# Kernel optimization log

Hardware: AMD Instinct MI355X
Metric: run time of the kernel (lower is better)

The kernel has to match this reference:

```python
import jax, jax.numpy as jnp
from jax import lax
import numpy as np

HEADS, SAMPLES = 4, 8
B, C, D, H, W = 1, 64, 16, 64, 64
HD = C // HEADS  # head_dim = 16
BN_EPS = 1e-5


def conv3d(x, w, b=None, pad=0):
    out = lax.conv_general_dilated(
        x, w, (1, 1, 1), [(pad, pad)] * 3,
        dimension_numbers=("NCDHW", "OIDHW", "NCDHW"))
    if b is not None:
        out = out + b[None, :, None, None, None]
    return out


def trilinear_sample(vol, grid):
    # vol: [Dv,Hv,Wv,Cc]; grid: [...,3] with torch grid_sample semantics:
    # grid[...,0] -> x (W axis), grid[...,1] -> y (H axis), grid[...,2] -> z (D axis)
    # align_corners=True, padding_mode='border'. Returns [..., Cc].
    Dv, Hv, Wv, _ = vol.shape
    ix = (grid[..., 0] + 1.0) * 0.5 * (Wv - 1)
    iy = (grid[..., 1] + 1.0) * 0.5 * (Hv - 1)
    iz = (grid[..., 2] + 1.0) * 0.5 * (Dv - 1)
    x0 = jnp.floor(ix); y0 = jnp.floor(iy); z0 = jnp.floor(iz)
    wx = (ix - x0)[..., None]; wy = (iy - y0)[..., None]; wz = (iz - z0)[..., None]
    x0i = jnp.clip(x0.astype(jnp.int32), 0, Wv - 1); x1i = jnp.clip(x0i + 1, 0, Wv - 1)
    y0i = jnp.clip(y0.astype(jnp.int32), 0, Hv - 1); y1i = jnp.clip(y0i + 1, 0, Hv - 1)
    z0i = jnp.clip(z0.astype(jnp.int32), 0, Dv - 1); z1i = jnp.clip(z0i + 1, 0, Dv - 1)
    g = lambda z, y, x: vol[z, y, x]
    out = (g(z0i, y0i, x0i) * (1 - wz) * (1 - wy) * (1 - wx)
           + g(z0i, y0i, x1i) * (1 - wz) * (1 - wy) * wx
           + g(z0i, y1i, x0i) * (1 - wz) * wy * (1 - wx)
           + g(z0i, y1i, x1i) * (1 - wz) * wy * wx
           + g(z1i, y0i, x0i) * wz * (1 - wy) * (1 - wx)
           + g(z1i, y0i, x1i) * wz * (1 - wy) * wx
           + g(z1i, y1i, x0i) * wz * wy * (1 - wx)
           + g(z1i, y1i, x1i) * wz * wy * wx)
    return out


def t_deform(feat_prev, feat_curr, p):
    b, c, d, h, w = feat_curr.shape
    kv = conv3d(feat_prev, p["kv_w"], p["kv_b"])          # [B,2C,D,H,W]
    q = conv3d(feat_curr, p["q_w"], p["q_b"])              # [B,C,D,H,W]
    # offset branch: conv3x3 -> GELU(exact) -> conv3x3(no bias) -> tanh
    o = conv3d(feat_curr, p["off1_w"], p["off1_b"], pad=1)
    o = jax.nn.gelu(o, approximate=False)
    o = jnp.tanh(conv3d(o, p["off2_w"], None, pad=1))      # [B,M*S*3,D,H,W]
    off = o.reshape(b, HEADS, SAMPLES, 3, d, h, w).transpose(0, 1, 4, 5, 6, 2, 3)  # [B,M,D,H,W,S,3]
    zz, yy, xx = jnp.meshgrid(jnp.linspace(-1, 1, d), jnp.linspace(-1, 1, h),
                              jnp.linspace(-1, 1, w), indexing="ij")
    base = jnp.stack((zz, yy, xx), axis=-1).astype(feat_curr.dtype)  # [D,H,W,3]
    scale = jnp.array([d, h, w], dtype=feat_curr.dtype)
    grid = base[None, None, :, :, :, None, :] + off / scale
    grid = jnp.clip(grid, -1.0, 1.0)
    grid = grid.transpose(0, 1, 5, 2, 3, 4, 6).reshape(b * HEADS, SAMPLES, d, h, w, 3)
    # channels-last per (batch,head) volume; avoids torch's explicit repeat over samples
    vols = kv.reshape(b, HEADS, 2 * HD, d, h, w).transpose(0, 1, 3, 4, 5, 2)
    vols = vols.reshape(b * HEADS, d, h, w, 2 * HD)
    sampled = jax.vmap(trilinear_sample)(vols, grid)        # [B*M,S,D,H,W,2*HD]
    sampled = sampled.reshape(b, HEADS, SAMPLES, d, h, w, 2 * HD)
    key, value = sampled[..., :HD], sampled[..., HD:]
    qh = q.reshape(b, HEADS, HD, d, h, w) * (HD ** -0.5)
    attn = jnp.einsum("bmcdhw,bmsdhwc->bmsdhw", qh, key)
    attn = jax.nn.softmax(attn, axis=2)
    fused = jnp.einsum("bmsdhw,bmsdhwc->bmcdhw", attn, value).reshape(b, c, d, h, w)
    out = conv3d(fused, p["out_w"], p["out_b"])
    # BatchNorm3d (eval: running stats) + ReLU
    inv = lax.rsqrt(p["bn_var"] + BN_EPS)
    out = (out - p["bn_mean"][None, :, None, None, None]) * (inv * p["bn_gamma"])[None, :, None, None, None] \
          + p["bn_beta"][None, :, None, None, None]
    return jax.nn.relu(out)


def setup_inputs() -> dict:
    key = jax.random.key(0)
    ks = jax.random.split(key, 16)
    r = lambda k, shp, s=0.05: (jax.random.normal(k, shp, dtype=jnp.float32) * s)
    return {
        "mid_feat": jax.random.normal(ks[0], (B, C, D, H, W), dtype=jnp.float32),
        "occ_feat": jax.random.normal(ks[1], (B, C, D, H, W), dtype=jnp.float32),
        "prev_feat": jax.random.normal(ks[2], (B, C, D, H, W), dtype=jnp.float32),
        "off1_w": r(ks[3], (C, C, 3, 3, 3)), "off1_b": r(ks[4], (C,)),
        "off2_w": r(ks[5], (HEADS * SAMPLES * 3, C, 3, 3, 3)),
        "kv_w": r(ks[6], (2 * C, C, 1, 1, 1)), "kv_b": r(ks[7], (2 * C,)),
        "q_w": r(ks[8], (C, C, 1, 1, 1)), "q_b": r(ks[9], (C,)),
        "out_w": r(ks[10], (C, C, 1, 1, 1)), "out_b": r(ks[11], (C,)),
        "bn_gamma": jnp.ones((C,), jnp.float32), "bn_beta": jnp.zeros((C,), jnp.float32),
        "bn_mean": jnp.zeros((C,), jnp.float32), "bn_var": jnp.ones((C,), jnp.float32),
    }


def reference(mid_feat, occ_feat, prev_feat, off1_w, off1_b, off2_w, kv_w, kv_b,
              q_w, q_b, out_w, out_b, bn_gamma, bn_beta, bn_mean, bn_var):
    p = dict(off1_w=off1_w, off1_b=off1_b, off2_w=off2_w, kv_w=kv_w, kv_b=kv_b,
             q_w=q_w, q_b=q_b, out_w=out_w, out_b=out_b, bn_gamma=bn_gamma,
             bn_beta=bn_beta, bn_mean=bn_mean, bn_var=bn_var)
    d1 = t_deform(mid_feat, occ_feat, p)
    d2 = t_deform(mid_feat, prev_feat, p)
    return jnp.concatenate([mid_feat, d1, d2], axis=1)  # [B,3C,D,H,W]
```

## Files before the change

kernel.cpp:

```cpp
#include <hip/hip_runtime.h>
#include <math.h>

#define DD 16
#define HH 64
#define WW 64
#define VV (DD*HH*WW)
#define CC 64
#define NHEADS 4
#define NSAMP 8
#define HDIM 16

typedef unsigned int uint;
typedef unsigned short ushort;
typedef __attribute__((ext_vector_type(8))) short bf16x8;
typedef __attribute__((ext_vector_type(4))) float f32x4;

__device__ __forceinline__ float clampf(float v, float lo, float hi){ return fminf(fmaxf(v, lo), hi); }
__device__ __forceinline__ int imin(int a, int b){ return a < b ? a : b; }
__device__ __forceinline__ int imax(int a, int b){ return a > b ? a : b; }

__device__ __forceinline__ ushort f2bf(float f){
  uint u = __float_as_uint(f);
  uint r = (u + 0x7fffu + ((u>>16)&1u)) >> 16;
  return (ushort)r;
}
__device__ __forceinline__ uint packbf2(float a, float b){
  return (uint)f2bf(a) | ((uint)f2bf(b) << 16);
}
__device__ __forceinline__ float bflo(uint u){ return __uint_as_float(u << 16); }
__device__ __forceinline__ float bfhi(uint u){ return __uint_as_float(u & 0xffff0000u); }
__device__ __forceinline__ float bf2f(ushort u){ return __uint_as_float((uint)u << 16); }

__device__ __forceinline__ float dot8(uint4 k, const float* q){
  return q[0]*bflo(k.x)+q[1]*bfhi(k.x)+q[2]*bflo(k.y)+q[3]*bfhi(k.y)
       + q[4]*bflo(k.z)+q[5]*bfhi(k.z)+q[6]*bflo(k.w)+q[7]*bfhi(k.w);
}
__device__ __forceinline__ void acc8(uint4 u, float cw, float* val){
  val[0]+=cw*bflo(u.x); val[1]+=cw*bfhi(u.x);
  val[2]+=cw*bflo(u.y); val[3]+=cw*bfhi(u.y);
  val[4]+=cw*bflo(u.z); val[5]+=cw*bfhi(u.z);
  val[6]+=cw*bflo(u.w); val[7]+=cw*bfhi(u.w);
}

__global__ void repack_wmfma(const float* __restrict__ w, uint* __restrict__ o, int MG){
  int U = blockIdx.x*256 + threadIdx.x;
  int total = 54*MG*256;
  if (U >= total) return;
  int j2 = U & 3;
  int m  = (U>>2) & 15;
  int q  = (U>>6) & 3;
  int rest = U >> 8;
  int g = rest % MG;
  int s = rest / MG;
  int tap = s >> 1, h = s & 1;
  int co = g*16 + m;
  int ci = h*32 + q*8 + j2*2;
  int base = co*1728 + ci*27 + tap;
  o[U] = packbf2(w[base], w[base + 27]);
}
__global__ void repack_w1mfma(const float* __restrict__ w, uint* __restrict__ o, int MT){
  int U = blockIdx.x*256 + threadIdx.x;
  int total = 2*MT*256;
  if (U >= total) return;
  int j2 = U & 3;
  int lane = (U>>2) & 63;
  int frag = U >> 8;
  int mt = frag % MT;
  int ks = frag / MT;
  int q = lane >> 4, m = lane & 15;
  int co = mt*16 + m;
  int ci = ks*32 + q*8 + j2*2;
  o[U] = packbf2(w[co*CC + ci], w[co*CC + ci + 1]);
}

template<int CO, int EPI>
__global__ __launch_bounds__(256) void conv1_mfma(
    const float* __restrict__ xa, const float* __restrict__ xb,
    const uint* __restrict__ wA, const float* __restrict__ bias,
    void* __restrict__ outp)
{
  constexpr int MT = CO/16;
  constexpr int MW = MT/4;
  __shared__ ushort xt[64*72];
  int tid = threadIdx.x;
  int lane = tid & 63;
  int g = __builtin_amdgcn_readfirstlane(tid >> 6);
  int q = lane >> 4, n = lane & 15;
  int call = blockIdx.x >> 10;
  int v0 = (blockIdx.x & 1023) * 64;
  const float* x = call ? xb : xa;
  for (int it = tid; it < 64*32; it += 256){
    int vox = it & 63; int cp = it >> 6;
    float a = x[(size_t)(2*cp)*VV + v0 + vox];
    float b = x[(size_t)(2*cp+1)*VV + v0 + vox];
    *reinterpret_cast<uint*>(&xt[vox*72 + 2*cp]) = packbf2(a,b);
  }
  __syncthreads();
  f32x4 acc[MW][4];
  #pragma unroll
  for (int mw=0;mw<MW;mw++)
    #pragma unroll
    for (int nt=0;nt<4;nt++){ acc[mw][nt].x=0.f; acc[mw][nt].y=0.f; acc[mw][nt].z=0.f; acc[mw][nt].w=0.f; }
  const char* ldsb = reinterpret_cast<const char*>(xt);
  const char* wac  = reinterpret_cast<const char*>(wA);
  #pragma unroll
  for (int ks=0; ks<2; ks++){
    bf16x8 bfr[4];
    #pragma unroll
    for (int nt=0; nt<4; nt++)
      bfr[nt] = *reinterpret_cast<const bf16x8*>(ldsb + ((nt*16+n)*144 + q*16 + ks*64));
    #pragma unroll
    for (int mw=0; mw<MW; mw++){
      int mt = g*MW + mw;
      bf16x8 af = *reinterpret_cast<const bf16x8*>(wac + (size_t)((ks*MT + mt)*64 + lane)*16);
      #pragma unroll
      for (int nt=0; nt<4; nt++)
        acc[mw][nt] = __builtin_amdgcn_mfma_f32_16x16x32_bf16(af, bfr[nt], acc[mw][nt], 0, 0, 0);
    }
  }
  #pragma unroll
  for (int mw=0; mw<MW; mw++){
    int mt = g*MW + mw;
    int cob = mt*16 + q*4;
    #pragma unroll
    for (int nt=0; nt<4; nt++){
      int v = v0 + nt*16 + n;
      float r0 = acc[mw][nt].x + bias[cob+0];
      float r1 = acc[mw][nt].y + bias[cob+1];
      float r2 = acc[mw][nt].z + bias[cob+2];
      float r3 = acc[mw][nt].w + bias[cob+3];
      if (EPI == 0){
        int z = v >> 12, y = (v >> 6) & 63, xx = v & 63;
        int head = cob >> 5;
        uint* vols = (uint*)outp;
        uint2 pk; pk.x = packbf2(r0,r1); pk.y = packbf2(r2,r3);
        *reinterpret_cast<uint2*>(vols + ((size_t)head*VV + (size_t)(y*WW+xx)*DD + z)*16 + ((cob&31)>>1)) = pk;
      } else {
        ushort* ob = (ushort*)outp + (size_t)call*CC*VV;
        uint2 pk; pk.x = packbf2(r0*0.25f, r1*0.25f); pk.y = packbf2(r2*0.25f, r3*0.25f);
        *reinterpret_cast<uint2*>(ob + (size_t)v*64 + cob) = pk;
      }
    }
  }
}

template<int CO, int INPK, int OUTPK>
__global__ __launch_bounds__(256) void conv3_mfma(
    const float* __restrict__ xa, const float* __restrict__ xb,
    const uint* __restrict__ xpk,
    const uint* __restrict__ wA, const float* __restrict__ bias,
    void* __restrict__ outp)
{
  constexpr int MG = CO/16;
  constexpr int MROW = CO/32;
  __shared__ ushort xh[300*40];
  int tid = threadIdx.x;
  int lane = tid & 63;
  int w = __builtin_amdgcn_readfirstlane(tid >> 6);
  int q = lane >> 4, n = lane & 15;
  int bid = blockIdx.x;
  int xcd = bid & 7, islot = bid >> 3;
  int call = islot >> 7;
  int z = xcd*2 + ((islot >> 6) & 1);
  int rem = islot & 63;
  int by = (rem >> 3) << 3, bx = (rem & 7) << 3;

  const float* xin = call ? xb : xa;
  const uint* xinp = xpk + (size_t)call*32*VV;

  int mbase = (w & 1) * MROW;
  int np = w >> 1;
  int lo[2];
  #pragma unroll
  for (int nt=0;nt<2;nt++){
    int vox = (np*2+nt)*16 + n;
    lo[nt] = ((vox>>3)*10 + (vox&7))*80 + q*16;
  }
  f32x4 acc[MROW][2];
  #pragma unroll
  for (int mr=0;mr<MROW;mr++)
    #pragma unroll
    for (int nt=0;nt<2;nt++){ acc[mr][nt].x=0.f; acc[mr][nt].y=0.f; acc[mr][nt].z=0.f; acc[mr][nt].w=0.f; }

  const char* ldsb = reinterpret_cast<const char*>(xh);
  const char* wac  = reinterpret_cast<const char*>(wA);

  #pragma unroll 1
  for (int h=0; h<2; h++){
    if (h) __syncthreads();
    for (int it = tid; it < 2400; it += 256){
      int cg = it / 300; int pos = it - cg*300;
      int dz = pos/100; int r = pos - dz*100; int dy = r/10; int dxx = r - dy*10;
      int gz = z + dz - 1, gy = by + dy - 1, gx = bx + dxx - 1;
      bool ok = (gz>=0 && gz<DD && gy>=0 && gy<HH && gx>=0 && gx<WW);
      uint2 pk; pk.x = 0u; pk.y = 0u;
      if (ok){
        size_t gv = (size_t)((gz*HH+gy)*WW + gx);
        if (INPK){
          int cp0 = h*16 + cg*2;
          pk.x = xinp[(size_t)cp0*VV + gv];
          pk.y = xinp[(size_t)(cp0+1)*VV + gv];
        } else {
          int ci0 = h*32 + cg*4;
          float v0 = xin[(size_t)(ci0  )*VV + gv];
          float v1 = xin[(size_t)(ci0+1)*VV + gv];
          float v2 = xin[(size_t)(ci0+2)*VV + gv];
          float v3 = xin[(size_t)(ci0+3)*VV + gv];
          pk.x = packbf2(v0,v1); pk.y = packbf2(v2,v3);
        }
      }
      *reinterpret_cast<uint2*>(&xh[pos*40 + cg*4]) = pk;
    }
    __syncthreads();
    #pragma unroll 3
    for (int tap=0; tap<27; tap++){
      int dz = tap/9; int r9 = tap - dz*9; int dy = r9/3; int dxx = r9 - dy*3;
      int stepOff = (dz*100 + dy*10 + dxx)*80;
      int s = tap*2 + h;
      bf16x8 af[MROW];
      #pragma unroll
      for (int mr=0;mr<MROW;mr++)
        af[mr] = *reinterpret_cast<const bf16x8*>(wac + (size_t)((s*MG + mbase+mr)*64 + lane)*16);
      bf16x8 bf[2];
      #pragma unroll
      for (int nt=0;nt<2;nt++)
        bf[nt] = *reinterpret_cast<const bf16x8*>(ldsb + (lo[nt] + stepOff));
      #pragma unroll
      for (int mr=0;mr<MROW;mr++)
        #pragma unroll
        for (int nt=0;nt<2;nt++)
          acc[mr][nt] = __builtin_amdgcn_mfma_f32_16x16x32_bf16(af[mr], bf[nt], acc[mr][nt], 0, 0, 0);
    }
  }

  #pragma unroll
  for (int mr=0; mr<MROW; mr++){
    int cob = (mbase+mr)*16 + q*4;
    #pragma unroll
    for (int nt=0; nt<2; nt++){
      int vox = (np*2+nt)*16 + n;
      int vy = by + (vox>>3), vx = bx + (vox&8-1);
      vy = by + (vox>>3); vx = bx + (vox&7);
      size_t gv = (size_t)((z*HH + vy)*WW + vx);
      float r0 = acc[mr][nt].x, r1 = acc[mr][nt].y, r2 = acc[mr][nt].z, r3 = acc[mr][nt].w;
      if (OUTPK == 1){
        r0 += bias[cob+0]; r1 += bias[cob+1]; r2 += bias[cob+2]; r3 += bias[cob+3];
        r0 = 0.5f*r0*(1.f + erff(r0*0.70710678118654752f));
        r1 = 0.5f*r1*(1.f + erff(r1*0.70710678118654752f));
        r2 = 0.5f*r2*(1.f + erff(r2*0.70710678118654752f));
        r3 = 0.5f*r3*(1.f + erff(r3*0.70710678118654752f));
        uint* dst = (uint*)outp + (size_t)call*32*VV;
        dst[(size_t)(cob>>1)*VV + gv]     = packbf2(r0,r1);
        dst[(size_t)((cob>>1)+1)*VV + gv] = packbf2(r2,r3);
      } else {
        ushort* dst = (ushort*)outp + (size_t)call*96*VV;
        uint2 pk;
        pk.x = packbf2(tanhf(r0), tanhf(r1));
        pk.y = packbf2(tanhf(r2), tanhf(r3));
        *reinterpret_cast<uint2*>(dst + (size_t)gv*96 + cob) = pk;
      }
    }
  }
}

struct Geom { int x0,x1,y0,y1,z0,z1; float wx,wy,wz; };
__device__ __forceinline__ Geom make_geom(float zb, float yb, float xb,
                                          float o0, float o1, float o2){
  float g0 = clampf(zb + o0*(1.f/16.f), -1.f, 1.f);
  float g1 = clampf(yb + o1*(1.f/64.f), -1.f, 1.f);
  float g2 = clampf(xb + o2*(1.f/64.f), -1.f, 1.f);
  float ix = (g0+1.f)*0.5f*63.f;
  float iy = (g1+1.f)*0.5f*63.f;
  float iz = (g2+1.f)*0.5f*15.f;
  float fx=floorf(ix), fy=floorf(iy), fz=floorf(iz);
  Geom g;
  g.wx = ix-fx; g.wy = iy-fy; g.wz = iz-fz;
  g.x0 = imin(imax((int)fx,0), WW-1); g.x1 = imin(g.x0+1, WW-1);
  g.y0 = imin(imax((int)fy,0), HH-1); g.y1 = imin(g.y0+1, HH-1);
  g.z0 = imin(imax((int)fz,0), DD-1); g.z1 = imin(g.z0+1, DD-1);
  return g;
}

__global__ __launch_bounds__(256) void sample_attn_kernel(
    const ushort* __restrict__ qbuf, const ushort* __restrict__ offbuf,
    const uint* __restrict__ vols, const uint* __restrict__ woA,
    const float* __restrict__ outb, const float* __restrict__ bng,
    const float* __restrict__ bnb, const float* __restrict__ bnm,
    const float* __restrict__ bnv, float* __restrict__ dout)
{
  __shared__ ushort fsb[16*72];
  int t = threadIdx.x;
  int lane = t & 63;
  int m = __builtin_amdgcn_readfirstlane(t >> 6);
  int slot = lane >> 2;
  int r = lane & 3;
  int bid = blockIdx.x;
  int xcd = bid & 7, islot = bid >> 3;
  int call = islot >> 9;
  int z = xcd*2 + ((islot >> 8) & 1);
  int rem = islot & 255;
  int y = rem >> 2;
  int x0 = (rem & 3) << 4;
  int x = x0 + slot;
  int vbase = (z*HH + y)*WW + x0;
  int v = vbase + slot;

  const ushort* qb = qbuf   + (size_t)call*CC*VV;
  const ushort* ob = offbuf + (size_t)call*96*VV;

  uint4 qu = *reinterpret_cast<const uint4*>(qb + (size_t)v*64 + m*16 + (r&1)*8);
  float qf[8];
  qf[0]=bflo(qu.x); qf[1]=bfhi(qu.x); qf[2]=bflo(qu.y); qf[3]=bfhi(qu.y);
  qf[4]=bflo(qu.z); qf[5]=bfhi(qu.z); qf[6]=bflo(qu.w); qf[7]=bfhi(qu.w);

  uint ou[12];
  {
    const uint4* op4 = reinterpret_cast<const uint4*>(ob + (size_t)v*96 + m*24);
    uint4 a = op4[0], b4 = op4[1], c4 = op4[2];
    ou[0]=a.x;  ou[1]=a.y;  ou[2]=a.z;  ou[3]=a.w;
    ou[4]=b4.x; ou[5]=b4.y; ou[6]=b4.z; ou[7]=b4.w;
    ou[8]=c4.x; ou[9]=c4.y; ou[10]=c4.z; ou[11]=c4.w;
  }

  float zbf = -1.f + (float)z*(2.f/15.f);
  float ybf = -1.f + (float)y*(2.f/63.f);
  float xbf = -1.f + (float)x*(2.f/63.f);

  const uint* vol = vols + (size_t)m*VV*16;
  float roleK = (r < 2) ? 1.f : 0.f;
  float lrun = 0.f;
  float fused[8];
  #pragma unroll
  for (int c=0;c<8;c++) fused[c]=0.f;

  #pragma unroll
  for (int s=0;s<NSAMP;s++){
    int i0 = 3*s, i1 = 3*s+1, i2 = 3*s+2;
    float o0 = (i0&1) ? bfhi(ou[i0>>1]) : bflo(ou[i0>>1]);
    float o1 = (i1&1) ? bfhi(ou[i1>>1]) : bflo(ou[i1>>1]);
    float o2 = (i2&1) ? bfhi(ou[i2>>1]) : bflo(ou[i2>>1]);
    Geom g = make_geom(zbf,ybf,xbf,o0,o1,o2);
    float acc[8];
    #pragma unroll
    for (int c=0;c<8;c++) acc[c]=0.f;
    #pragma unroll
    for (int ky=0;ky<2;ky++)
    #pragma unroll
    for (int kx=0;kx<2;kx++){
      int cy = ky? g.y1:g.y0, cx = kx? g.x1:g.x0;
      float wyx = (ky? g.wy : 1.f-g.wy)*(kx? g.wx : 1.f-g.wx);
      const uint* rowp = vol + (size_t)((cy*WW + cx)*DD)*16;
      #pragma unroll
      for (int kz=0;kz<2;kz++){
        int cz = kz? g.z1:g.z0;
        float cw = wyx * (kz? g.wz : 1.f-g.wz);
        uint4 u = reinterpret_cast<const uint4*>(rowp + (size_t)cz*16)[r];
        acc8(u, cw, acc);
      }
    }
    float h = qf[0]*acc[0]+qf[1]*acc[1]+qf[2]*acc[2]+qf[3]*acc[3]
            + qf[4]*acc[4]+qf[5]*acc[5]+qf[6]*acc[6]+qf[7]*acc[7];
    h *= roleK;
    h += __shfl_xor(h, 1);
    h += __shfl_xor(h, 2);
    float e = expf(h);
    lrun += e;
    #pragma unroll
    for (int c=0;c<8;c++) fused[c] += e*acc[c];
  }
  float isum = 1.f/lrun;
  if (r >= 2){
    uint4 pk;
    pk.x = packbf2(fused[0]*isum, fused[1]*isum);
    pk.y = packbf2(fused[2]*isum, fused[3]*isum);
    pk.z = packbf2(fused[4]*isum, fused[5]*isum);
    pk.w = packbf2(fused[6]*isum, fused[7]*isum);
    *reinterpret_cast<uint4*>(&fsb[slot*72 + m*16 + (r&1)*8]) = pk;
  }
  __syncthreads();

  int qq = lane >> 4, n = lane & 15;
  f32x4 acco;
  acco.x=0.f; acco.y=0.f; acco.z=0.f; acco.w=0.f;
  const char* ldsb = reinterpret_cast<const char*>(fsb);
  const char* wac  = reinterpret_cast<const char*>(woA);
  #pragma unroll
  for (int ks=0; ks<2; ks++){
    bf16x8 af = *reinterpret_cast<const bf16x8*>(wac + (size_t)((ks*4 + m)*64 + lane)*16);
    bf16x8 bfv = *reinterpret_cast<const bf16x8*>(ldsb + (n*144 + qq*16 + ks*64));
    acco = __builtin_amdgcn_mfma_f32_16x16x32_bf16(af, bfv, acco, 0, 0, 0);
  }
  int choff = 64 + call*64;
  #pragma unroll
  for (int rr=0; rr<4; rr++){
    int co = m*16 + qq*4 + rr;
    float inv = rsqrtf(bnv[co] + 1e-5f) * bng[co];
    float val = (acco[rr] + outb[co] - bnm[co]) * inv + bnb[co];
    val = fmaxf(val, 0.f);
    dout[(size_t)(choff+co)*VV + vbase + n] = val;
  }
}

extern "C" void kernel_launch(void* const* d_in, const int* in_sizes, int n_in,
                              void* d_out, int out_size, void* d_ws, size_t ws_size,
                              hipStream_t stream){
  (void)in_sizes; (void)n_in; (void)out_size; (void)ws_size;
  const float* mid  = (const float*)d_in[0];
  const float* occ  = (const float*)d_in[1];
  const float* prev = (const float*)d_in[2];
  const float* off1w= (const float*)d_in[3];
  const float* off1b= (const float*)d_in[4];
  const float* off2w= (const float*)d_in[5];
  const float* kvw  = (const float*)d_in[6];
  const float* kvb  = (const float*)d_in[7];
  const float* qw   = (const float*)d_in[8];
  const float* qb   = (const float*)d_in[9];
  const float* outw = (const float*)d_in[10];
  const float* outb = (const float*)d_in[11];
  const float* bng  = (const float*)d_in[12];
  const float* bnb  = (const float*)d_in[13];
  const float* bnm  = (const float*)d_in[14];
  const float* bnv  = (const float*)d_in[15];
  float* out = (float*)d_out;

  uint*   vols  = (uint*)d_ws;
  ushort* qbuf  = (ushort*)(vols + (size_t)4*VV*16);
  uint*   o1pk  = (uint*)(qbuf + (size_t)2*CC*VV);
  ushort* offb  = (ushort*)(o1pk + (size_t)2*32*VV);
  uint*   wA1   = (uint*)(offb + (size_t)2*96*VV);
  uint*   wA2   = wA1 + 55296;
  uint*   wo    = wA2 + 82944;
  uint*   wkv   = wo  + 2048;
  uint*   wq    = wkv + 4096;

  repack_wmfma<<<(55296+255)/256, 256, 0, stream>>>(off1w, wA1, 4);
  repack_wmfma<<<(82944+255)/256, 256, 0, stream>>>(off2w, wA2, 6);
  repack_w1mfma<<<8, 256, 0, stream>>>(outw, wo, 4);
  repack_w1mfma<<<16, 256, 0, stream>>>(kvw, wkv, 8);
  repack_w1mfma<<<8, 256, 0, stream>>>(qw, wq, 4);
  conv1_mfma<128,0><<<1024, 256, 0, stream>>>(mid, mid, wkv, kvb, (void*)vols);
  hipMemcpyAsync(out, mid, (size_t)CC*VV*sizeof(float), hipMemcpyDeviceToDevice, stream);
  conv1_mfma<64,1><<<2048, 256, 0, stream>>>(occ, prev, wq, qb, (void*)qbuf);
  conv3_mfma<64,0,1><<<2048, 256, 0, stream>>>(occ, prev, (const uint*)nullptr, wA1, off1b, (void*)o1pk);
  conv3_mfma<96,1,0><<<2048, 256, 0, stream>>>((const float*)nullptr, (const float*)nullptr, o1pk, wA2, off1b, (void*)offb);
  sample_attn_kernel<<<8192, 256, 0, stream>>>(qbuf, offb, vols, wo,
      outb, bng, bnb, bnm, bnv, out);
}
```

Before: 376.4 us.

## Stage conv epilogues through LDS for coalesced stores and use bf16 dot2 trilinear gather

The q-projection and offset-conv epilogues now write tiles into shared memory and then emit fully coalesced 16-byte global stores, replacing the scattered 8-byte stores. In the deformable sampling kernel, the z-pair of corner loads is combined with packed bf16 weights via perm plus v_dot2_f32_bf16, which cuts the FMA count in half. tanh and exp switch to fast __expf-based versions. The cost is extra LDS round trips and syncs, plus lower precision from bf16-rounded interpolation weights and the approximate transcendentals.

```diff
diff --git a/kernel.cpp b/kernel.cpp
--- a/kernel.cpp
+++ b/kernel.cpp
@@ -31,15 +31,9 @@
 __device__ __forceinline__ float bfhi(uint u){ return __uint_as_float(u & 0xffff0000u); }
 __device__ __forceinline__ float bf2f(ushort u){ return __uint_as_float((uint)u << 16); }
 
-__device__ __forceinline__ float dot8(uint4 k, const float* q){
-  return q[0]*bflo(k.x)+q[1]*bfhi(k.x)+q[2]*bflo(k.y)+q[3]*bfhi(k.y)
-       + q[4]*bflo(k.z)+q[5]*bfhi(k.z)+q[6]*bflo(k.w)+q[7]*bfhi(k.w);
-}
-__device__ __forceinline__ void acc8(uint4 u, float cw, float* val){
-  val[0]+=cw*bflo(u.x); val[1]+=cw*bfhi(u.x);
-  val[2]+=cw*bflo(u.y); val[3]+=cw*bfhi(u.y);
-  val[4]+=cw*bflo(u.z); val[5]+=cw*bfhi(u.z);
-  val[6]+=cw*bflo(u.w); val[7]+=cw*bfhi(u.w);
+__device__ __forceinline__ float fast_tanh(float x){
+  float e = __expf(2.f*x);
+  return 1.f - 2.f/(e + 1.f);
 }
 
 __global__ void repack_wmfma(const float* __restrict__ w, uint* __restrict__ o, int MG){
@@ -118,28 +112,44 @@
         acc[mw][nt] = __builtin_amdgcn_mfma_f32_16x16x32_bf16(af, bfr[nt], acc[mw][nt], 0, 0, 0);
     }
   }
-  #pragma unroll
-  for (int mw=0; mw<MW; mw++){
-    int mt = g*MW + mw;
-    int cob = mt*16 + q*4;
-    #pragma unroll
-    for (int nt=0; nt<4; nt++){
-      int v = v0 + nt*16 + n;
-      float r0 = acc[mw][nt].x + bias[cob+0];
-      float r1 = acc[mw][nt].y + bias[cob+1];
-      float r2 = acc[mw][nt].z + bias[cob+2];
-      float r3 = acc[mw][nt].w + bias[cob+3];
-      if (EPI == 0){
+  if (EPI == 0){
+    #pragma unroll
+    for (int mw=0; mw<MW; mw++){
+      int mt = g*MW + mw;
+      int cob = mt*16 + q*4;
+      #pragma unroll
+      for (int nt=0; nt<4; nt++){
+        int v = v0 + nt*16 + n;
+        float r0 = acc[mw][nt].x + bias[cob+0];
+        float r1 = acc[mw][nt].y + bias[cob+1];
+        float r2 = acc[mw][nt].z + bias[cob+2];
+        float r3 = acc[mw][nt].w + bias[cob+3];
         int z = v >> 12, y = (v >> 6) & 63, xx = v & 63;
         int head = cob >> 5;
         uint* vols = (uint*)outp;
         uint2 pk; pk.x = packbf2(r0,r1); pk.y = packbf2(r2,r3);
         *reinterpret_cast<uint2*>(vols + ((size_t)head*VV + (size_t)(y*WW+xx)*DD + z)*16 + ((cob&31)>>1)) = pk;
-      } else {
-        ushort* ob = (ushort*)outp + (size_t)call*CC*VV;
-        uint2 pk; pk.x = packbf2(r0*0.25f, r1*0.25f); pk.y = packbf2(r2*0.25f, r3*0.25f);
-        *reinterpret_cast<uint2*>(ob + (size_t)v*64 + cob) = pk;
       }
+    }
+  } else {
+    __syncthreads();
+    ushort* xr = xt;
+    int cob = g*16 + q*4;
+    #pragma unroll
+    for (int nt=0; nt<4; nt++){
+      int vox = nt*16 + n;
+      uint2 pk;
+      pk.x = packbf2((acc[0][nt].x + bias[cob+0])*0.25f, (acc[0][nt].y + bias[cob+1])*0.25f);
+      pk.y = packbf2((acc[0][nt].z + bias[cob+2])*0.25f, (acc[0][nt].w + bias[cob+3])*0.25f);
+      *reinterpret_cast<uint2*>(&xr[vox*64 + cob]) = pk;
+    }
+    __syncthreads();
+    char* ob = (char*)((ushort*)outp + (size_t)call*CC*VV) + (size_t)v0*128;
+    const char* lb = reinterpret_cast<const char*>(xr);
+    #pragma unroll
+    for (int k=0; k<2; k++){
+      int idx = tid + k*256;
+      *reinterpret_cast<uint4*>(ob + idx*16) = *reinterpret_cast<const uint4*>(lb + idx*16);
     }
   }
 }
@@ -233,18 +243,19 @@
     }
   }
 
-  #pragma unroll
-  for (int mr=0; mr<MROW; mr++){
-    int cob = (mbase+mr)*16 + q*4;
-    #pragma unroll
-    for (int nt=0; nt<2; nt++){
-      int vox = (np*2+nt)*16 + n;
-      int vy = by + (vox>>3), vx = bx + (vox&8-1);
-      vy = by + (vox>>3); vx = bx + (vox&7);
-      size_t gv = (size_t)((z*HH + vy)*WW + vx);
-      float r0 = acc[mr][nt].x, r1 = acc[mr][nt].y, r2 = acc[mr][nt].z, r3 = acc[mr][nt].w;
-      if (OUTPK == 1){
-        r0 += bias[cob+0]; r1 += bias[cob+1]; r2 += bias[cob+2]; r3 += bias[cob+3];
+  if (OUTPK == 1){
+    #pragma unroll
+    for (int mr=0; mr<MROW; mr++){
+      int cob = (mbase+mr)*16 + q*4;
+      #pragma unroll
+      for (int nt=0; nt<2; nt++){
+        int vox = (np*2+nt)*16 + n;
+        int vy = by + (vox>>3), vx = bx + (vox&7);
+        size_t gv = (size_t)((z*HH + vy)*WW + vx);
+        float r0 = acc[mr][nt].x + bias[cob+0];
+        float r1 = acc[mr][nt].y + bias[cob+1];
+        float r2 = acc[mr][nt].z + bias[cob+2];
+        float r3 = acc[mr][nt].w + bias[cob+3];
         r0 = 0.5f*r0*(1.f + erff(r0*0.70710678118654752f));
         r1 = 0.5f*r1*(1.f + erff(r1*0.70710678118654752f));
         r2 = 0.5f*r2*(1.f + erff(r2*0.70710678118654752f));
@@ -252,13 +263,33 @@
         uint* dst = (uint*)outp + (size_t)call*32*VV;
         dst[(size_t)(cob>>1)*VV + gv]     = packbf2(r0,r1);
         dst[(size_t)((cob>>1)+1)*VV + gv] = packbf2(r2,r3);
-      } else {
-        ushort* dst = (ushort*)outp + (size_t)call*96*VV;
+      }
+    }
+  } else {
+    __syncthreads();
+    ushort* xr = xh;
+    #pragma unroll
+    for (int mr=0; mr<MROW; mr++){
+      int cob = (mbase+mr)*16 + q*4;
+      #pragma unroll
+      for (int nt=0; nt<2; nt++){
+        int vox = (np*2+nt)*16 + n;
         uint2 pk;
-        pk.x = packbf2(tanhf(r0), tanhf(r1));
-        pk.y = packbf2(tanhf(r2), tanhf(r3));
-        *reinterpret_cast<uint2*>(dst + (size_t)gv*96 + cob) = pk;
+        pk.x = packbf2(fast_tanh(acc[mr][nt].x), fast_tanh(acc[mr][nt].y));
+        pk.y = packbf2(fast_tanh(acc[mr][nt].z), fast_tanh(acc[mr][nt].w));
+        *reinterpret_cast<uint2*>(&xr[vox*96 + cob]) = pk;
       }
+    }
+    __syncthreads();
+    ushort* dst = (ushort*)outp + (size_t)call*96*VV;
+    const char* lb = reinterpret_cast<const char*>(xr);
+    #pragma unroll
+    for (int k=0; k<3; k++){
+      int idx = tid + k*256;
+      int row = idx/96;
+      int off = idx - row*96;
+      size_t gb = (size_t)((z*HH + by + row)*WW + bx)*192 + (size_t)off*16;
+      *reinterpret_cast<uint4*>((char*)dst + gb) = *reinterpret_cast<const uint4*>(lb + idx*16);
     }
   }
 }
@@ -326,7 +357,7 @@
   float ybf = -1.f + (float)y*(2.f/63.f);
   float xbf = -1.f + (float)x*(2.f/63.f);
 
-  const uint* vol = vols + (size_t)m*VV*16;
+  const char* volb = reinterpret_cast<const char*>(vols) + (size_t)m*VV*64;
   float roleK = (r < 2) ? 1.f : 0.f;
   float lrun = 0.f;
   float fused[8];
@@ -340,6 +371,11 @@
     float o1 = (i1&1) ? bfhi(ou[i1>>1]) : bflo(ou[i1>>1]);
     float o2 = (i2&1) ? bfhi(ou[i2>>1]) : bflo(ou[i2>>1]);
     Geom g = make_geom(zbf,ybf,xbf,o0,o1,o2);
+    int tz0 = g.z0*64 + r*16;
+    int tz1 = g.z1*64 + r*16;
+    float wx1 = g.wx, wx0 = 1.f-g.wx;
+    float wy1 = g.wy, wy0 = 1.f-g.wy;
+    float wz1 = g.wz, wz0 = 1.f-g.wz;
     float acc[8];
     #pragma unroll
     for (int c=0;c<8;c++) acc[c]=0.f;
@@ -348,22 +384,38 @@
     #pragma unroll
     for (int kx=0;kx<2;kx++){
       int cy = ky? g.y1:g.y0, cx = kx? g.x1:g.x0;
-      float wyx = (ky? g.wy : 1.f-g.wy)*(kx? g.wx : 1.f-g.wx);
-      const uint* rowp = vol + (size_t)((cy*WW + cx)*DD)*16;
-      #pragma unroll
-      for (int kz=0;kz<2;kz++){
-        int cz = kz? g.z1:g.z0;
-        float cw = wyx * (kz? g.wz : 1.f-g.wz);
-        uint4 u = reinterpret_cast<const uint4*>(rowp + (size_t)cz*16)[r];
-        acc8(u, cw, acc);
-      }
+      float wyx = (ky? wy1:wy0)*(kx? wx1:wx0);
+      float a0 = wyx*wz0, a1 = wyx*wz1;
+      uint wzp;
+      asm("v_cvt_pk_bf16_f32 %0, %1, %2" : "=v"(wzp) : "v"(a0), "v"(a1));
+      int tb = ((cy<<6) + cx) << 10;
+      const char* p = volb + tb;
+      uint4 u0 = *reinterpret_cast<const uint4*>(p + tz0);
+      uint4 u1 = *reinterpret_cast<const uint4*>(p + tz1);
+      uint plo, phi;
+      plo = __builtin_amdgcn_perm(u1.x, u0.x, 0x05040100u);
+      phi = __builtin_amdgcn_perm(u1.x, u0.x, 0x07060302u);
+      asm("v_dot2_f32_bf16 %0, %1, %2, %0" : "+v"(acc[0]) : "v"(plo), "v"(wzp));
+      asm("v_dot2_f32_bf16 %0, %1, %2, %0" : "+v"(acc[1]) : "v"(phi), "v"(wzp));
+      plo = __builtin_amdgcn_perm(u1.y, u0.y, 0x05040100u);
+      phi = __builtin_amdgcn_perm(u1.y, u0.y, 0x07060302u);
+      asm("v_dot2_f32_bf16 %0, %1, %2, %0" : "+v"(acc[2]) : "v"(plo), "v"(wzp));
+      asm("v_dot2_f32_bf16 %0, %1, %2, %0" : "+v"(acc[3]) : "v"(phi), "v"(wzp));
+      plo = __builtin_amdgcn_perm(u1.z, u0.z, 0x05040100u);
+      phi = __builtin_amdgcn_perm(u1.z, u0.z, 0x07060302u);
+      asm("v_dot2_f32_bf16 %0, %1, %2, %0" : "+v"(acc[4]) : "v"(plo), "v"(wzp));
+      asm("v_dot2_f32_bf16 %0, %1, %2, %0" : "+v"(acc[5]) : "v"(phi), "v"(wzp));
+      plo = __builtin_amdgcn_perm(u1.w, u0.w, 0x05040100u);
+      phi = __builtin_amdgcn_perm(u1.w, u0.w, 0x07060302u);
+      asm("v_dot2_f32_bf16 %0, %1, %2, %0" : "+v"(acc[6]) : "v"(plo), "v"(wzp));
+      asm("v_dot2_f32_bf16 %0, %1, %2, %0" : "+v"(acc[7]) : "v"(phi), "v"(wzp));
     }
     float h = qf[0]*acc[0]+qf[1]*acc[1]+qf[2]*acc[2]+qf[3]*acc[3]
             + qf[4]*acc[4]+qf[5]*acc[5]+qf[6]*acc[6]+qf[7]*acc[7];
     h *= roleK;
     h += __shfl_xor(h, 1);
     h += __shfl_xor(h, 2);
-    float e = expf(h);
+    float e = __expf(h);
     lrun += e;
     #pragma unroll
     for (int c=0;c<8;c++) fused[c] += e*acc[c];
```

Measured after the change: 363.3 us. -3.5%, faster.
